# Optimization experiments

Measured on AMD Instinct MI355X. Metric: run time of the kernel, lower is better.

## Reference

```python
import jax, jax.numpy as jnp
import numpy as np

B, N, C, H = 2, 4096, 256, 4
EPS = 1e-12  # torch F.normalize eps


def setup_inputs() -> dict:
    key = jax.random.key(0)
    k1, k2, k3, k4 = jax.random.split(key, 4)
    x = jax.random.normal(k1, (B, N, C), dtype=jnp.float32)
    w_qkv = jax.random.normal(k2, (3 * C, C), dtype=jnp.float32) * (1.0 / np.sqrt(C))
    w_out = jax.random.normal(k3, (C, C), dtype=jnp.float32) * (1.0 / np.sqrt(C))
    b_out = jnp.zeros((C,), dtype=jnp.float32)
    temperature = jnp.ones((H, 1, 1), dtype=jnp.float32)
    return {"x": x, "w_qkv": w_qkv, "w_out": w_out, "b_out": b_out,
            "temperature": temperature}


def _l2norm(t):
    # torch.nn.functional.normalize(t, dim=-1): t / max(||t||_2, eps)
    n = jnp.sqrt(jnp.sum(t * t, axis=-1, keepdims=True))
    return t / jnp.maximum(n, EPS)


def reference(x, w_qkv, w_out, b_out, temperature):
    b, n, c = x.shape
    d = c // H
    qkv = x @ w_qkv.T                                   # [B,N,3C]
    qkv = qkv.reshape(b, n, 3, H, d).transpose(2, 0, 3, 1, 4)  # [3,B,H,N,d]
    q, k, v = qkv[0], qkv[1], qkv[2]                    # each [B,H,N,d]
    # transpose(-2,-1) -> [B,H,d,N]; normalize along N (per channel over tokens)
    q = _l2norm(jnp.swapaxes(q, -2, -1))                # [B,H,d,N]
    k = _l2norm(jnp.swapaxes(k, -2, -1))                # [B,H,d,N]
    v = jnp.swapaxes(v, -2, -1)                         # [B,H,d,N]
    # attn[n,m] = sum_d q[d,n] * k[d,m], scaled by learned per-head temperature
    attn = jnp.einsum('bhdn,bhdm->bhnm', q, k) * temperature  # [B,H,N,N]
    attn = jax.nn.softmax(attn, axis=-1)
    # (attn @ v^T): [B,H,N,N] @ [B,H,N,d] -> [B,H,N,d]
    out = jnp.einsum('bhnm,bhdm->bhnd', attn, v)        # [B,H,N,d]
    # faithful to source: permute(0,3,1,2) -> [B,d,H,N], then reshape(B,N,C)
    out = out.transpose(0, 3, 1, 2).reshape(b, n, c)
    return out @ w_out.T + b_out
```

## Files before the change

### kernel.cpp

```cpp
#include <hip/hip_runtime.h>

typedef _Float16 f16;
typedef f16 f16x8 __attribute__((ext_vector_type(8)));
typedef f16 f16x4 __attribute__((ext_vector_type(4)));
typedef __fp16 fp16x2 __attribute__((ext_vector_type(2)));
typedef float f32x4 __attribute__((ext_vector_type(4)));
typedef float f32x16 __attribute__((ext_vector_type(16)));
typedef unsigned int u32;

#define NTOK 4096

#define GLL(gsrc, ldst) \
  __builtin_amdgcn_global_load_lds( \
      (const __attribute__((address_space(1))) void*)(gsrc), \
      (__attribute__((address_space(3))) void*)(ldst), 16, 0, 0)

__global__ __launch_bounds__(256) void k_cvt(
    const float* __restrict__ x, const float* __restrict__ wq,
    const float* __restrict__ wo,
    f16* __restrict__ xb, f16* __restrict__ wqb, f16* __restrict__ wob)
{
  const int bx = blockIdx.x;
  const float* src; f16* dst; int off;
  if (bx < 2048)      { src = x;  dst = xb;  off = bx * 1024; }
  else if (bx < 2240) { src = wq; dst = wqb; off = (bx - 2048) * 1024; }
  else                { src = wo; dst = wob; off = (bx - 2240) * 1024; }
  const int i = off + threadIdx.x * 4;
  float4 f = *(const float4*)(src + i);
  f16x4 h;
  h[0] = (f16)f.x; h[1] = (f16)f.y; h[2] = (f16)f.z; h[3] = (f16)f.w;
  *(f16x4*)(dst + i) = h;
}

__global__ __launch_bounds__(256) void k_gemm(
    const f16* __restrict__ A, const f16* __restrict__ W,
    int K, int mode,
    f16* __restrict__ Qb, f16* __restrict__ Kb, f16* __restrict__ Vtb,
    float* __restrict__ outF, const float* __restrict__ bias,
    float* __restrict__ partQ, float* __restrict__ partK)
{
  __shared__ f16 Al[64 * 40];
  __shared__ f16 Wl[64 * 40];
  __shared__ float redl[4][64];
  const int t = threadIdx.x;
  const int w = t >> 6, l = t & 63;
  const int lrow = l & 15, lk = l >> 4;
  const int m0 = blockIdx.y * 64, nc0 = blockIdx.x * 64;
  f32x4 acc[4] = {};
  const int srow = t >> 2, sseg = t & 3;
  for (int k0 = 0; k0 < K; k0 += 32) {
    __syncthreads();
    f16x8 av = *(const f16x8*)(A + (size_t)(m0 + srow) * K + k0 + sseg * 8);
    f16x8 wv = *(const f16x8*)(W + (size_t)(nc0 + srow) * K + k0 + sseg * 8);
    *(f16x8*)(Al + srow * 40 + sseg * 8) = av;
    *(f16x8*)(Wl + srow * 40 + sseg * 8) = wv;
    __syncthreads();
    f16x8 af = *(const f16x8*)(Al + (w * 16 + lrow) * 40 + lk * 8);
#pragma unroll
    for (int ct = 0; ct < 4; ++ct) {
      f16x8 bf = *(const f16x8*)(Wl + (ct * 16 + lrow) * 40 + lk * 8);
      acc[ct] = __builtin_amdgcn_mfma_f32_16x16x32_f16(af, bf, acc[ct], 0, 0, 0);
    }
  }
  const int nb = m0 + w * 16 + lk * 4;
  if (mode == 0) {
    const int b = nb >> 12, n = nb & 4095;
#pragma unroll
    for (int ct = 0; ct < 4; ++ct) {
      int gc = nc0 + ct * 16 + lrow;
      int s = gc >> 8, h = (gc >> 6) & 3, dd = gc & 63;
      int bh = b * 4 + h;
      if (s == 2) {
        f16x4 v;
#pragma unroll
        for (int j = 0; j < 4; ++j) v[j] = (f16)acc[ct][j];
        *(f16x4*)(Vtb + ((size_t)bh * 64 + dd) * 4096 + n) = v;
      } else {
        f16* dst = (s == 0) ? Qb : Kb;
#pragma unroll
        for (int j = 0; j < 4; ++j)
          dst[((size_t)bh * 4096 + n + j) * 64 + dd] = (f16)acc[ct][j];
      }
    }
    if (nc0 < 512) {
#pragma unroll
      for (int ct = 0; ct < 4; ++ct) {
        float v = acc[ct][0] * acc[ct][0] + acc[ct][1] * acc[ct][1]
                + acc[ct][2] * acc[ct][2] + acc[ct][3] * acc[ct][3];
        v += __shfl_xor(v, 16, 64);
        v += __shfl_xor(v, 32, 64);
        if (lk == 0) redl[w][ct * 16 + lrow] = v;
      }
      __syncthreads();
      if (t < 64) {
        float sq = redl[0][t] + redl[1][t] + redl[2][t] + redl[3][t];
        const int s = nc0 >> 8, h2 = (nc0 >> 6) & 3;
        const int b2 = m0 >> 12, mb = (m0 >> 6) & 63;
        float* dst = (s == 0) ? partQ : partK;
        dst[((b2 * 4 + h2) * 64 + mb) * 64 + t] = sq;
      }
    }
  } else {
#pragma unroll
    for (int ct = 0; ct < 4; ++ct) {
      int gc = nc0 + ct * 16 + lrow;
      float bv = bias[gc];
#pragma unroll
      for (int j = 0; j < 4; ++j)
        outF[(size_t)(nb + j) * 256 + gc] = acc[ct][j] + bv;
    }
  }
}

__global__ __launch_bounds__(512) void k_norm2(
    const float* __restrict__ partQ, const float* __restrict__ partK,
    const float* __restrict__ temp, f16* __restrict__ cqh)
{
  const int t = threadIdx.x;
  const int bh = t >> 6, dd = t & 63;
  float sq = 0.f, sk = 0.f;
  for (int s = 0; s < 64; ++s) {
    sq += partQ[(bh * 64 + s) * 64 + dd];
    sk += partK[(bh * 64 + s) * 64 + dd];
  }
  float c = temp[bh & 3] * 1.4426950408889634f /
            (fmaxf(sqrtf(sq), 1e-12f) * fmaxf(sqrtf(sk), 1e-12f));
  cqh[t] = (f16)c;
}

__device__ inline void plane_swap(u32& a, u32& b) {
  asm volatile("v_permlane32_swap_b32 %0, %1" : "+v"(a), "+v"(b));
}

__global__ __launch_bounds__(512, 4) void k_flash6(
    const f16* __restrict__ Qb, const f16* __restrict__ Kb,
    const f16* __restrict__ Vtb, const f16* __restrict__ cqh,
    f16* __restrict__ Y)
{
  __shared__ f16 KVl[32768];
  __shared__ float Lsh[256];
  const int t = threadIdx.x, w = t >> 6, l = t & 63;
  const int r = l & 31, hi = l >> 5;
  const int ks = w >> 1, qh = w & 1;
  const int r7 = r & 7;
  int nb2 = (blockIdx.x & 7) * 64 + (blockIdx.x >> 3);
  const int bh = nb2 >> 6, qt = nb2 & 63;
  const size_t base = (size_t)bh * NTOK * 64;
  f16x8 qf0, qf1, qf2, qf3;
  {
    const f16* cq = cqh + bh * 64;
    const f16* qp = Qb + base + (size_t)(qt * 64 + qh * 32 + r) * 64 + hi * 8;
    qf0 = *(const f16x8*)(qp)      * *(const f16x8*)(cq +  0 + hi * 8);
    qf1 = *(const f16x8*)(qp + 16) * *(const f16x8*)(cq + 16 + hi * 8);
    qf2 = *(const f16x8*)(qp + 32) * *(const f16x8*)(cq + 32 + hi * 8);
    qf3 = *(const f16x8*)(qp + 48) * *(const f16x8*)(cq + 48 + hi * 8);
  }
  const f16* srcK = Kb + base + (size_t)(w * 8 + (l >> 3)) * 64 + ((l & 7) ^ (l >> 3)) * 8;
  const int vrow = w * 4 + (l >> 4);
  const f16* srcV = Vtb + base + (size_t)vrow * 4096 + ((l & 15) ^ (vrow & 7)) * 8;
  const int dK = w * 8 * 64;
  const int dV = 8192 + w * 4 * 128;
#define STAGE(cur, tile) { \
    const f16* sk_ = srcK + (size_t)(tile) * 8192; \
    const f16* sv_ = srcV + (tile) * 128; \
    GLL(sk_,          KVl + (cur) * 16384 + dK); \
    GLL(sk_ + 4096,   KVl + (cur) * 16384 + dK + 4096); \
    GLL(sv_,          KVl + (cur) * 16384 + dV); \
    GLL(sv_ + 131072, KVl + (cur) * 16384 + dV + 4096); }
  const int kro = (ks * 32 + r) * 64;
  const int kc0 = ((0 + hi) ^ r7) * 8, kc1 = ((2 + hi) ^ r7) * 8;
  const int kc2 = ((4 + hi) ^ r7) * 8, kc3 = ((6 + hi) ^ r7) * 8;
  const int vb0 = 8192 + r * 128, vb1 = 8192 + (32 + r) * 128;
  const int vc0 = ((ks * 4 + 0 + hi) ^ r7) * 8, vc1 = ((ks * 4 + 2 + hi) ^ r7) * 8;

  f32x16 oacc0 = {}, oacc1 = {};
  float lsw = 0.f;
  STAGE(0, 0);
  __syncthreads();
  for (int tl = 0; tl < 32; ++tl) {
    const int cur = tl & 1;
    const f16* Bb = KVl + cur * 16384;
    f16x8 kf0 = *(const f16x8*)(Bb + kro + kc0);
    f16x8 kf1 = *(const f16x8*)(Bb + kro + kc1);
    f16x8 kf2 = *(const f16x8*)(Bb + kro + kc2);
    f16x8 kf3 = *(const f16x8*)(Bb + kro + kc3);
    f16x8 vf0 = *(const f16x8*)(Bb + vb0 + vc0);
    f16x8 vf1 = *(const f16x8*)(Bb + vb0 + vc1);
    f16x8 vf2 = *(const f16x8*)(Bb + vb1 + vc0);
    f16x8 vf3 = *(const f16x8*)(Bb + vb1 + vc1);
    if (tl < 31) STAGE(cur ^ 1, tl + 1);
    f32x16 sacc = {};
    __builtin_amdgcn_s_setprio(1);
    sacc = __builtin_amdgcn_mfma_f32_32x32x16_f16(kf0, qf0, sacc, 0, 0, 0);
    sacc = __builtin_amdgcn_mfma_f32_32x32x16_f16(kf1, qf1, sacc, 0, 0, 0);
    sacc = __builtin_amdgcn_mfma_f32_32x32x16_f16(kf2, qf2, sacc, 0, 0, 0);
    sacc = __builtin_amdgcn_mfma_f32_32x32x16_f16(kf3, qf3, sacc, 0, 0, 0);
    __builtin_amdgcn_s_setprio(0);
    u32 Dw[8];
#pragma unroll
    for (int u = 0; u < 4; ++u) {
#pragma unroll
      for (int v = 0; v < 2; ++v) {
        float a  = __builtin_amdgcn_exp2f(sacc[u * 4 + v * 2]);
        float b2 = __builtin_amdgcn_exp2f(sacc[u * 4 + v * 2 + 1]);
        lsw += a + b2;
        union { fp16x2 h; u32 u; } cv;
        cv.h = __builtin_amdgcn_cvt_pkrtz(a, b2);
        Dw[u * 2 + v] = cv.u;
      }
    }
    plane_swap(Dw[0], Dw[2]);
    plane_swap(Dw[1], Dw[3]);
    plane_swap(Dw[4], Dw[6]);
    plane_swap(Dw[5], Dw[7]);
    union { f16x8 v; u32 d[4]; } p0, p1;
    p0.d[0] = Dw[0]; p0.d[1] = Dw[1]; p0.d[2] = Dw[2]; p0.d[3] = Dw[3];
    p1.d[0] = Dw[4]; p1.d[1] = Dw[5]; p1.d[2] = Dw[6]; p1.d[3] = Dw[7];
    __builtin_amdgcn_s_setprio(1);
    oacc0 = __builtin_amdgcn_mfma_f32_32x32x16_f16(p0.v, vf0, oacc0, 0, 0, 0);
    oacc0 = __builtin_amdgcn_mfma_f32_32x32x16_f16(p1.v, vf1, oacc0, 0, 0, 0);
    oacc1 = __builtin_amdgcn_mfma_f32_32x32x16_f16(p0.v, vf2, oacc1, 0, 0, 0);
    oacc1 = __builtin_amdgcn_mfma_f32_32x32x16_f16(p1.v, vf3, oacc1, 0, 0, 0);
    __builtin_amdgcn_s_setprio(0);
    __syncthreads();
  }
#undef STAGE
  lsw += __shfl_xor(lsw, 32, 64);
  if (hi == 0) Lsh[w * 32 + r] = lsw;
#pragma unroll
  for (int dt = 0; dt < 2; ++dt) {
    f16* orow = KVl + w * 2048 + (dt * 32 + r) * 32;
    const f32x16& oa = dt ? oacc1 : oacc0;
#pragma unroll
    for (int u = 0; u < 4; ++u) {
      f16x4 h4;
      h4[0] = (f16)oa[u * 4 + 0]; h4[1] = (f16)oa[u * 4 + 1];
      h4[2] = (f16)oa[u * 4 + 2]; h4[3] = (f16)oa[u * 4 + 3];
      *(f16x4*)(orow + ((u ^ (r & 3)) * 8) + hi * 4) = h4;
    }
  }
  __syncthreads();
  const int s2 = w >> 2, dt2 = (w >> 1) & 1, qh2 = w & 1;
  const int g = s2 * 2 + hi;
  const int b = bh >> 2, h = bh & 3;
  float accv[8] = {}, denv[8] = {};
#pragma unroll
  for (int ksl = 0; ksl < 4; ++ksl) {
    const int wp = ksl * 2 + qh2;
    f16x8 rd = *(const f16x8*)(KVl + wp * 2048 + (dt2 * 32 + r) * 32 + ((g ^ (r & 3)) * 8));
    f32x4 la = *(const f32x4*)(Lsh + wp * 32 + g * 8);
    f32x4 lb = *(const f32x4*)(Lsh + wp * 32 + g * 8 + 4);
#pragma unroll
    for (int j = 0; j < 4; ++j) {
      accv[j]     += (float)rd[j];
      accv[4 + j] += (float)rd[4 + j];
      denv[j]     += la[j];
      denv[4 + j] += lb[j];
    }
  }
  const int ng = qt * 64 + qh2 * 32 + g * 8;
  const int np = (dt2 * 32 + r) * 64 + h * 16 + (ng >> 8);
  const int cp_ = ng & 255;
  f16x8 yv;
#pragma unroll
  for (int j = 0; j < 8; ++j) yv[j] = (f16)(accv[j] / denv[j]);
  *(f16x8*)(Y + ((size_t)b * 4096 + np) * 256 + cp_) = yv;
}

extern "C" void kernel_launch(void* const* d_in, const int* in_sizes, int n_in,
                              void* d_out, int out_size, void* d_ws, size_t ws_size,
                              hipStream_t stream)
{
  const float* x     = (const float*)d_in[0];
  const float* w_qkv = (const float*)d_in[1];
  const float* w_out = (const float*)d_in[2];
  const float* b_out = (const float*)d_in[3];
  const float* temp  = (const float*)d_in[4];

  char* ws = (char*)d_ws;
  f16*   xb    = (f16*)(ws);
  f16*   wqkvb = (f16*)(ws + 4 * 1024 * 1024);
  f16*   woutb = (f16*)(ws + 4 * 1024 * 1024 + 512 * 1024);
  f16*   Qb    = (f16*)(ws + 5  * 1024 * 1024);
  f16*   Kb    = (f16*)(ws + 9  * 1024 * 1024);
  f16*   Vtb   = (f16*)(ws + 13 * 1024 * 1024);
  f16*   cqh   = (f16*)(ws + 17 * 1024 * 1024);
  float* partQ = (float*)(ws + 17 * 1024 * 1024 + 8192);
  float* partK = (float*)(ws + 17 * 1024 * 1024 + 8192 + 131072);
  f16*   Y     = (f16*)(ws + 18 * 1024 * 1024);
  float* outF  = (float*)d_out;

  k_cvt<<<2304, 256, 0, stream>>>(x, w_qkv, w_out, xb, wqkvb, woutb);
  k_gemm<<<dim3(12, 128), 256, 0, stream>>>(xb, wqkvb, 256, 0, Qb, Kb, Vtb,
                                            nullptr, nullptr, partQ, partK);
  k_norm2<<<1, 512, 0, stream>>>(partQ, partK, temp, cqh);
  k_flash6<<<512, 512, 0, stream>>>(Qb, Kb, Vtb, cqh, Y);
  k_gemm<<<dim3(4, 128), 256, 0, stream>>>(Y, woutb, 256, 1, nullptr, nullptr, nullptr,
                                           outF, b_out, nullptr, nullptr);
}
```

Baseline: 83.27 us.

## Fuse x fp16 conversion into QKV GEMM and load V directly from global

The standalone conversion of x to fp16 is removed. The QKV GEMM now reads fp32 x and converts it in registers, which saves one kernel pass and an intermediate buffer. The flash kernel no longer stages V tiles through LDS: each lane loads its V fragments straight from global memory every iteration, which halves LDS use per block. This trades LDS traffic and occupancy pressure for uncoalesced or latency-exposed global loads of V inside the main loop.

```diff
diff --git a/kernel.cpp b/kernel.cpp
--- a/kernel.cpp
+++ b/kernel.cpp
@@ -16,15 +16,13 @@
       (__attribute__((address_space(3))) void*)(ldst), 16, 0, 0)
 
 __global__ __launch_bounds__(256) void k_cvt(
-    const float* __restrict__ x, const float* __restrict__ wq,
-    const float* __restrict__ wo,
-    f16* __restrict__ xb, f16* __restrict__ wqb, f16* __restrict__ wob)
+    const float* __restrict__ wq, const float* __restrict__ wo,
+    f16* __restrict__ wqb, f16* __restrict__ wob)
 {
   const int bx = blockIdx.x;
   const float* src; f16* dst; int off;
-  if (bx < 2048)      { src = x;  dst = xb;  off = bx * 1024; }
-  else if (bx < 2240) { src = wq; dst = wqb; off = (bx - 2048) * 1024; }
-  else                { src = wo; dst = wob; off = (bx - 2240) * 1024; }
+  if (bx < 192) { src = wq; dst = wqb; off = bx * 1024; }
+  else          { src = wo; dst = wob; off = (bx - 192) * 1024; }
   const int i = off + threadIdx.x * 4;
   float4 f = *(const float4*)(src + i);
   f16x4 h;
@@ -33,7 +31,7 @@
 }
 
 __global__ __launch_bounds__(256) void k_gemm(
-    const f16* __restrict__ A, const f16* __restrict__ W,
+    const void* __restrict__ Araw, const f16* __restrict__ W,
     int K, int mode,
     f16* __restrict__ Qb, f16* __restrict__ Kb, f16* __restrict__ Vtb,
     float* __restrict__ outF, const float* __restrict__ bias,
@@ -50,7 +48,16 @@
   const int srow = t >> 2, sseg = t & 3;
   for (int k0 = 0; k0 < K; k0 += 32) {
     __syncthreads();
-    f16x8 av = *(const f16x8*)(A + (size_t)(m0 + srow) * K + k0 + sseg * 8);
+    f16x8 av;
+    if (mode == 0) {
+      const float* ap = (const float*)Araw + (size_t)(m0 + srow) * K + k0 + sseg * 8;
+      float4 a0 = *(const float4*)(ap);
+      float4 a1 = *(const float4*)(ap + 4);
+      av[0] = (f16)a0.x; av[1] = (f16)a0.y; av[2] = (f16)a0.z; av[3] = (f16)a0.w;
+      av[4] = (f16)a1.x; av[5] = (f16)a1.y; av[6] = (f16)a1.z; av[7] = (f16)a1.w;
+    } else {
+      av = *(const f16x8*)((const f16*)Araw + (size_t)(m0 + srow) * K + k0 + sseg * 8);
+    }
     f16x8 wv = *(const f16x8*)(W + (size_t)(nc0 + srow) * K + k0 + sseg * 8);
     *(f16x8*)(Al + srow * 40 + sseg * 8) = av;
     *(f16x8*)(Wl + srow * 40 + sseg * 8) = wv;
@@ -132,12 +139,12 @@
   asm volatile("v_permlane32_swap_b32 %0, %1" : "+v"(a), "+v"(b));
 }
 
-__global__ __launch_bounds__(512, 4) void k_flash6(
+__global__ __launch_bounds__(512, 4) void k_flash8(
     const f16* __restrict__ Qb, const f16* __restrict__ Kb,
     const f16* __restrict__ Vtb, const f16* __restrict__ cqh,
     f16* __restrict__ Y)
 {
-  __shared__ f16 KVl[32768];
+  __shared__ f16 KVl[16384];
   __shared__ float Lsh[256];
   const int t = threadIdx.x, w = t >> 6, l = t & 63;
   const int r = l & 31, hi = l >> 5;
@@ -156,22 +163,15 @@
     qf3 = *(const f16x8*)(qp + 48) * *(const f16x8*)(cq + 48 + hi * 8);
   }
   const f16* srcK = Kb + base + (size_t)(w * 8 + (l >> 3)) * 64 + ((l & 7) ^ (l >> 3)) * 8;
-  const int vrow = w * 4 + (l >> 4);
-  const f16* srcV = Vtb + base + (size_t)vrow * 4096 + ((l & 15) ^ (vrow & 7)) * 8;
-  const int dK = w * 8 * 64;
-  const int dV = 8192 + w * 4 * 128;
+  const int dK = w * 512;
 #define STAGE(cur, tile) { \
     const f16* sk_ = srcK + (size_t)(tile) * 8192; \
-    const f16* sv_ = srcV + (tile) * 128; \
-    GLL(sk_,          KVl + (cur) * 16384 + dK); \
-    GLL(sk_ + 4096,   KVl + (cur) * 16384 + dK + 4096); \
-    GLL(sv_,          KVl + (cur) * 16384 + dV); \
-    GLL(sv_ + 131072, KVl + (cur) * 16384 + dV + 4096); }
+    GLL(sk_,        KVl + (cur) * 8192 + dK); \
+    GLL(sk_ + 4096, KVl + (cur) * 8192 + dK + 4096); }
   const int kro = (ks * 32 + r) * 64;
   const int kc0 = ((0 + hi) ^ r7) * 8, kc1 = ((2 + hi) ^ r7) * 8;
   const int kc2 = ((4 + hi) ^ r7) * 8, kc3 = ((6 + hi) ^ r7) * 8;
-  const int vb0 = 8192 + r * 128, vb1 = 8192 + (32 + r) * 128;
-  const int vc0 = ((ks * 4 + 0 + hi) ^ r7) * 8, vc1 = ((ks * 4 + 2 + hi) ^ r7) * 8;
+  const f16* vp = Vtb + base + (size_t)r * 4096 + (ks * 4 + hi) * 8;
 
   f32x16 oacc0 = {}, oacc1 = {};
   float lsw = 0.f;
@@ -179,15 +179,16 @@
   __syncthreads();
   for (int tl = 0; tl < 32; ++tl) {
     const int cur = tl & 1;
-    const f16* Bb = KVl + cur * 16384;
+    const f16* vt = vp + tl * 128;
+    f16x8 vf0 = *(const f16x8*)(vt);
+    f16x8 vf1 = *(const f16x8*)(vt + 16);
+    f16x8 vf2 = *(const f16x8*)(vt + 32 * 4096);
+    f16x8 vf3 = *(const f16x8*)(vt + 32 * 4096 + 16);
+    const f16* Bb = KVl + cur * 8192;
     f16x8 kf0 = *(const f16x8*)(Bb + kro + kc0);
     f16x8 kf1 = *(const f16x8*)(Bb + kro + kc1);
     f16x8 kf2 = *(const f16x8*)(Bb + kro + kc2);
     f16x8 kf3 = *(const f16x8*)(Bb + kro + kc3);
-    f16x8 vf0 = *(const f16x8*)(Bb + vb0 + vc0);
-    f16x8 vf1 = *(const f16x8*)(Bb + vb0 + vc1);
-    f16x8 vf2 = *(const f16x8*)(Bb + vb1 + vc0);
-    f16x8 vf3 = *(const f16x8*)(Bb + vb1 + vc1);
     if (tl < 31) STAGE(cur ^ 1, tl + 1);
     f32x16 sacc = {};
     __builtin_amdgcn_s_setprio(1);
@@ -278,7 +279,6 @@
   const float* temp  = (const float*)d_in[4];
 
   char* ws = (char*)d_ws;
-  f16*   xb    = (f16*)(ws);
   f16*   wqkvb = (f16*)(ws + 4 * 1024 * 1024);
   f16*   woutb = (f16*)(ws + 4 * 1024 * 1024 + 512 * 1024);
   f16*   Qb    = (f16*)(ws + 5  * 1024 * 1024);
@@ -290,11 +290,11 @@
   f16*   Y     = (f16*)(ws + 18 * 1024 * 1024);
   float* outF  = (float*)d_out;
 
-  k_cvt<<<2304, 256, 0, stream>>>(x, w_qkv, w_out, xb, wqkvb, woutb);
-  k_gemm<<<dim3(12, 128), 256, 0, stream>>>(xb, wqkvb, 256, 0, Qb, Kb, Vtb,
+  k_cvt<<<256, 256, 0, stream>>>(w_qkv, w_out, wqkvb, woutb);
+  k_gemm<<<dim3(12, 128), 256, 0, stream>>>(x, wqkvb, 256, 0, Qb, Kb, Vtb,
                                             nullptr, nullptr, partQ, partK);
   k_norm2<<<1, 512, 0, stream>>>(partQ, partK, temp, cqh);
-  k_flash6<<<512, 512, 0, stream>>>(Qb, Kb, Vtb, cqh, Y);
+  k_flash8<<<512, 512, 0, stream>>>(Qb, Kb, Vtb, cqh, Y);
   k_gemm<<<dim3(4, 128), 256, 0, stream>>>(Y, woutb, 256, 1, nullptr, nullptr, nullptr,
                                            outF, b_out, nullptr, nullptr);
 }
```

New measurement: 109.3 us. +31.2%, slower.

## Fuse x fp32-to-fp16 conversion into larger-tile QKV GEMM with async weight loads

Applied to the files above, without the earlier changes.

The QKV projection now reads x in fp32 directly and converts it to fp16 while staging to shared memory. This removes the separate conversion pass and the xb workspace round trip. The QKV GEMM also moves to 128x128 tiles with 4x4 MFMA fragments per wave and swizzled global_load_lds for the weight tile, which cuts the number of blocks and raises reuse. The partial norm buffers shrink to 32 row-blocks, and the output projection gets its own specialized kernel. The trade-off is higher register pressure and fewer blocks in the QKV GEMM.

```diff
diff --git a/kernel.cpp b/kernel.cpp
--- a/kernel.cpp
+++ b/kernel.cpp
@@ -16,15 +16,13 @@
       (__attribute__((address_space(3))) void*)(ldst), 16, 0, 0)
 
 __global__ __launch_bounds__(256) void k_cvt(
-    const float* __restrict__ x, const float* __restrict__ wq,
-    const float* __restrict__ wo,
-    f16* __restrict__ xb, f16* __restrict__ wqb, f16* __restrict__ wob)
+    const float* __restrict__ wq, const float* __restrict__ wo,
+    f16* __restrict__ wqb, f16* __restrict__ wob)
 {
   const int bx = blockIdx.x;
   const float* src; f16* dst; int off;
-  if (bx < 2048)      { src = x;  dst = xb;  off = bx * 1024; }
-  else if (bx < 2240) { src = wq; dst = wqb; off = (bx - 2048) * 1024; }
-  else                { src = wo; dst = wob; off = (bx - 2240) * 1024; }
+  if (bx < 192) { src = wq; dst = wqb; off = bx * 1024; }
+  else          { src = wo; dst = wob; off = (bx - 192) * 1024; }
   const int i = off + threadIdx.x * 4;
   float4 f = *(const float4*)(src + i);
   f16x4 h;
@@ -32,82 +30,109 @@
   *(f16x4*)(dst + i) = h;
 }
 
-__global__ __launch_bounds__(256) void k_gemm(
-    const f16* __restrict__ A, const f16* __restrict__ W,
-    int K, int mode,
+__global__ __launch_bounds__(256, 2) void k_qkv(
+    const float* __restrict__ x, const f16* __restrict__ W,
     f16* __restrict__ Qb, f16* __restrict__ Kb, f16* __restrict__ Vtb,
-    float* __restrict__ outF, const float* __restrict__ bias,
     float* __restrict__ partQ, float* __restrict__ partK)
 {
-  __shared__ f16 Al[64 * 40];
-  __shared__ f16 Wl[64 * 40];
+  __shared__ f16 Al[128 * 40];
+  __shared__ f16 Wl[128 * 32];
   __shared__ float redl[4][64];
   const int t = threadIdx.x;
   const int w = t >> 6, l = t & 63;
   const int lrow = l & 15, lk = l >> 4;
-  const int m0 = blockIdx.y * 64, nc0 = blockIdx.x * 64;
-  f32x4 acc[4] = {};
-  const int srow = t >> 2, sseg = t & 3;
-  for (int k0 = 0; k0 < K; k0 += 32) {
-    __syncthreads();
-    f16x8 av = *(const f16x8*)(A + (size_t)(m0 + srow) * K + k0 + sseg * 8);
-    f16x8 wv = *(const f16x8*)(W + (size_t)(nc0 + srow) * K + k0 + sseg * 8);
-    *(f16x8*)(Al + srow * 40 + sseg * 8) = av;
-    *(f16x8*)(Wl + srow * 40 + sseg * 8) = wv;
-    __syncthreads();
-    f16x8 af = *(const f16x8*)(Al + (w * 16 + lrow) * 40 + lk * 8);
-#pragma unroll
-    for (int ct = 0; ct < 4; ++ct) {
-      f16x8 bf = *(const f16x8*)(Wl + (ct * 16 + lrow) * 40 + lk * 8);
-      acc[ct] = __builtin_amdgcn_mfma_f32_16x16x32_f16(af, bf, acc[ct], 0, 0, 0);
-    }
-  }
-  const int nb = m0 + w * 16 + lk * 4;
-  if (mode == 0) {
-    const int b = nb >> 12, n = nb & 4095;
-#pragma unroll
-    for (int ct = 0; ct < 4; ++ct) {
-      int gc = nc0 + ct * 16 + lrow;
-      int s = gc >> 8, h = (gc >> 6) & 3, dd = gc & 63;
-      int bh = b * 4 + h;
+  const int wm = w >> 1, wn = w & 1;
+  const int m0 = blockIdx.y * 128, nc0 = blockIdx.x * 128;
+  const int ar = t >> 1, aseg = t & 1;
+  const float* asrc = x + (size_t)(m0 + ar) * 256 + aseg * 16;
+  f16* adst = Al + ar * 40 + aseg * 16;
+  const int wrow = w * 32 + (l >> 2), wc = l & 3;
+  const f16* srcW1 = W + (size_t)(nc0 + wrow) * 256 + ((wc ^ (wrow & 3)) * 8);
+  const f16* srcW2 = W + (size_t)(nc0 + wrow + 16) * 256 + ((wc ^ (wrow & 3)) * 8);
+  f16* dstW1 = Wl + w * 1024;
+  f16* dstW2 = Wl + w * 1024 + 512;
+  f32x4 acc[4][4] = {};
+  for (int k0 = 0; k0 < 256; k0 += 32) {
+    __syncthreads();
+    GLL(srcW1 + k0, dstW1);
+    GLL(srcW2 + k0, dstW2);
+    {
+      const float* ap = asrc + k0;
+      float4 a0 = *(const float4*)(ap);
+      float4 a1 = *(const float4*)(ap + 4);
+      float4 a2 = *(const float4*)(ap + 8);
+      float4 a3 = *(const float4*)(ap + 12);
+      f16x8 h0, h1;
+      h0[0] = (f16)a0.x; h0[1] = (f16)a0.y; h0[2] = (f16)a0.z; h0[3] = (f16)a0.w;
+      h0[4] = (f16)a1.x; h0[5] = (f16)a1.y; h0[6] = (f16)a1.z; h0[7] = (f16)a1.w;
+      h1[0] = (f16)a2.x; h1[1] = (f16)a2.y; h1[2] = (f16)a2.z; h1[3] = (f16)a2.w;
+      h1[4] = (f16)a3.x; h1[5] = (f16)a3.y; h1[6] = (f16)a3.z; h1[7] = (f16)a3.w;
+      *(f16x8*)(adst) = h0;
+      *(f16x8*)(adst + 8) = h1;
+    }
+    __syncthreads();
+    f16x8 wf[4];
+#pragma unroll
+    for (int fc = 0; fc < 4; ++fc) {
+      const int row = wn * 64 + fc * 16 + lrow;
+      wf[fc] = *(const f16x8*)(Wl + row * 32 + ((lk ^ (row & 3)) * 8));
+    }
+#pragma unroll
+    for (int fr = 0; fr < 4; ++fr) {
+      f16x8 af = *(const f16x8*)(Al + (wm * 64 + fr * 16 + lrow) * 40 + lk * 8);
+#pragma unroll
+      for (int fc = 0; fc < 4; ++fc)
+        acc[fr][fc] = __builtin_amdgcn_mfma_f32_16x16x32_f16(af, wf[fc], acc[fr][fc], 0, 0, 0);
+    }
+  }
+  const int b = m0 >> 12, nbb = m0 & 4095;
+#pragma unroll
+  for (int fc = 0; fc < 4; ++fc) {
+    const int gc = nc0 + wn * 64 + fc * 16 + lrow;
+    const int s = gc >> 8, h = (gc >> 6) & 3, dd = gc & 63;
+    const int bh = b * 4 + h;
+#pragma unroll
+    for (int fr = 0; fr < 4; ++fr) {
+      const int n = nbb + wm * 64 + fr * 16 + lk * 4;
       if (s == 2) {
         f16x4 v;
 #pragma unroll
-        for (int j = 0; j < 4; ++j) v[j] = (f16)acc[ct][j];
+        for (int j = 0; j < 4; ++j) v[j] = (f16)acc[fr][fc][j];
         *(f16x4*)(Vtb + ((size_t)bh * 64 + dd) * 4096 + n) = v;
       } else {
         f16* dst = (s == 0) ? Qb : Kb;
 #pragma unroll
         for (int j = 0; j < 4; ++j)
-          dst[((size_t)bh * 4096 + n + j) * 64 + dd] = (f16)acc[ct][j];
+          dst[((size_t)bh * 4096 + n + j) * 64 + dd] = (f16)acc[fr][fc][j];
       }
     }
-    if (nc0 < 512) {
-#pragma unroll
-      for (int ct = 0; ct < 4; ++ct) {
-        float v = acc[ct][0] * acc[ct][0] + acc[ct][1] * acc[ct][1]
-                + acc[ct][2] * acc[ct][2] + acc[ct][3] * acc[ct][3];
-        v += __shfl_xor(v, 16, 64);
-        v += __shfl_xor(v, 32, 64);
-        if (lk == 0) redl[w][ct * 16 + lrow] = v;
+  }
+  if (nc0 < 512) {
+    float vsum[4] = {};
+#pragma unroll
+    for (int fc = 0; fc < 4; ++fc) {
+#pragma unroll
+      for (int fr = 0; fr < 4; ++fr) {
+        float v = acc[fr][fc][0] * acc[fr][fc][0] + acc[fr][fc][1] * acc[fr][fc][1]
+                + acc[fr][fc][2] * acc[fr][fc][2] + acc[fr][fc][3] * acc[fr][fc][3];
+        vsum[fc] += v;
       }
-      __syncthreads();
-      if (t < 64) {
-        float sq = redl[0][t] + redl[1][t] + redl[2][t] + redl[3][t];
-        const int s = nc0 >> 8, h2 = (nc0 >> 6) & 3;
-        const int b2 = m0 >> 12, mb = (m0 >> 6) & 63;
-        float* dst = (s == 0) ? partQ : partK;
-        dst[((b2 * 4 + h2) * 64 + mb) * 64 + t] = sq;
-      }
-    }
-  } else {
-#pragma unroll
-    for (int ct = 0; ct < 4; ++ct) {
-      int gc = nc0 + ct * 16 + lrow;
-      float bv = bias[gc];
-#pragma unroll
-      for (int j = 0; j < 4; ++j)
-        outF[(size_t)(nb + j) * 256 + gc] = acc[ct][j] + bv;
+      vsum[fc] += __shfl_xor(vsum[fc], 16, 64);
+      vsum[fc] += __shfl_xor(vsum[fc], 32, 64);
+    }
+    __syncthreads();
+    if (lk == 0) {
+#pragma unroll
+      for (int fc = 0; fc < 4; ++fc) redl[w][fc * 16 + lrow] = vsum[fc];
+    }
+    __syncthreads();
+    if (t < 128) {
+      const int wn2 = t >> 6, dd = t & 63;
+      const float sq = redl[wn2][dd] + redl[2 + wn2][dd];
+      const int h = ((nc0 >> 6) & 3) + wn2;
+      const int mb = (m0 >> 7) & 31;
+      float* dst = (nc0 >> 8) == 0 ? partQ : partK;
+      dst[((b * 4 + h) * 32 + mb) * 64 + dd] = sq;
     }
   }
 }
@@ -119,9 +144,9 @@
   const int t = threadIdx.x;
   const int bh = t >> 6, dd = t & 63;
   float sq = 0.f, sk = 0.f;
-  for (int s = 0; s < 64; ++s) {
-    sq += partQ[(bh * 64 + s) * 64 + dd];
-    sk += partK[(bh * 64 + s) * 64 + dd];
+  for (int s = 0; s < 32; ++s) {
+    sq += partQ[(bh * 32 + s) * 64 + dd];
+    sk += partK[(bh * 32 + s) * 64 + dd];
   }
   float c = temp[bh & 3] * 1.4426950408889634f /
             (fmaxf(sqrtf(sq), 1e-12f) * fmaxf(sqrtf(sk), 1e-12f));
@@ -158,8 +183,8 @@
   const f16* srcK = Kb + base + (size_t)(w * 8 + (l >> 3)) * 64 + ((l & 7) ^ (l >> 3)) * 8;
   const int vrow = w * 4 + (l >> 4);
   const f16* srcV = Vtb + base + (size_t)vrow * 4096 + ((l & 15) ^ (vrow & 7)) * 8;
-  const int dK = w * 8 * 64;
-  const int dV = 8192 + w * 4 * 128;
+  const int dK = w * 512;
+  const int dV = 8192 + w * 512;
 #define STAGE(cur, tile) { \
     const f16* sk_ = srcK + (size_t)(tile) * 8192; \
     const f16* sv_ = srcV + (tile) * 128; \
@@ -267,6 +292,43 @@
   *(f16x8*)(Y + ((size_t)b * 4096 + np) * 256 + cp_) = yv;
 }
 
+__global__ __launch_bounds__(256) void k_out(
+    const f16* __restrict__ A, const f16* __restrict__ W,
+    float* __restrict__ outF, const float* __restrict__ bias)
+{
+  __shared__ f16 Al[64 * 40];
+  __shared__ f16 Wl[64 * 40];
+  const int t = threadIdx.x;
+  const int w = t >> 6, l = t & 63;
+  const int lrow = l & 15, lk = l >> 4;
+  const int m0 = blockIdx.y * 64, nc0 = blockIdx.x * 64;
+  f32x4 acc[4] = {};
+  const int srow = t >> 2, sseg = t & 3;
+  for (int k0 = 0; k0 < 256; k0 += 32) {
+    __syncthreads();
+    f16x8 av = *(const f16x8*)(A + (size_t)(m0 + srow) * 256 + k0 + sseg * 8);
+    f16x8 wv = *(const f16x8*)(W + (size_t)(nc0 + srow) * 256 + k0 + sseg * 8);
+    *(f16x8*)(Al + srow * 40 + sseg * 8) = av;
+    *(f16x8*)(Wl + srow * 40 + sseg * 8) = wv;
+    __syncthreads();
+    f16x8 af = *(const f16x8*)(Al + (w * 16 + lrow) * 40 + lk * 8);
+#pragma unroll
+    for (int ct = 0; ct < 4; ++ct) {
+      f16x8 bf = *(const f16x8*)(Wl + (ct * 16 + lrow) * 40 + lk * 8);
+      acc[ct] = __builtin_amdgcn_mfma_f32_16x16x32_f16(af, bf, acc[ct], 0, 0, 0);
+    }
+  }
+  const int nb = m0 + w * 16 + lk * 4;
+#pragma unroll
+  for (int ct = 0; ct < 4; ++ct) {
+    int gc = nc0 + ct * 16 + lrow;
+    float bv = bias[gc];
+#pragma unroll
+    for (int j = 0; j < 4; ++j)
+      outF[(size_t)(nb + j) * 256 + gc] = acc[ct][j] + bv;
+  }
+}
+
 extern "C" void kernel_launch(void* const* d_in, const int* in_sizes, int n_in,
                               void* d_out, int out_size, void* d_ws, size_t ws_size,
                               hipStream_t stream)
@@ -278,7 +340,6 @@
   const float* temp  = (const float*)d_in[4];
 
   char* ws = (char*)d_ws;
-  f16*   xb    = (f16*)(ws);
   f16*   wqkvb = (f16*)(ws + 4 * 1024 * 1024);
   f16*   woutb = (f16*)(ws + 4 * 1024 * 1024 + 512 * 1024);
   f16*   Qb    = (f16*)(ws + 5  * 1024 * 1024);
@@ -290,11 +351,9 @@
   f16*   Y     = (f16*)(ws + 18 * 1024 * 1024);
   float* outF  = (float*)d_out;
 
-  k_cvt<<<2304, 256, 0, stream>>>(x, w_qkv, w_out, xb, wqkvb, woutb);
-  k_gemm<<<dim3(12, 128), 256, 0, stream>>>(xb, wqkvb, 256, 0, Qb, Kb, Vtb,
-                                            nullptr, nullptr, partQ, partK);
+  k_cvt<<<256, 256, 0, stream>>>(w_qkv, w_out, wqkvb, woutb);
+  k_qkv<<<dim3(6, 64), 256, 0, stream>>>(x, wqkvb, Qb, Kb, Vtb, partQ, partK);
   k_norm2<<<1, 512, 0, stream>>>(partQ, partK, temp, cqh);
   k_flash6<<<512, 512, 0, stream>>>(Qb, Kb, Vtb, cqh, Y);
-  k_gemm<<<dim3(4, 128), 256, 0, stream>>>(Y, woutb, 256, 1, nullptr, nullptr, nullptr,
-                                           outF, b_out, nullptr, nullptr);
-}
+  k_out<<<dim3(4, 128), 256, 0, stream>>>(Y, woutb, outF, b_out);
+}
```

Measured after the change: 98.77 us. 18.6% more time.
